# Performance work log

Hardware: AMD Instinct MI355X
Metric: run time of the kernel (lower is better)

Reference implementation:

```python
import jax, jax.numpy as jnp
import numpy as np
from jax import lax

B, T, D = 2048, 300, 40
H = 64          # BasicLSTMCell num_units
D1 = 128        # dense1 units
OUT = 512       # out_dim (num speakers)
FORGET_BIAS = 1.0
BN_EPS = 1e-3   # tf.layers.BatchNormalization default


def setup_inputs() -> dict:
    key = jax.random.key(0)
    ks = jax.random.split(key, 10)
    X = jax.random.normal(ks[0], (B, T, D), dtype=jnp.float32)
    seq_length = jax.random.randint(ks[1], (B,), 1, T + 1).astype(jnp.int32)
    # BasicLSTMCell kernel: [input_dim + H, 4H], gate order i, j, f, o
    lstm_kernel = jax.random.normal(ks[2], (D + H, 4 * H), dtype=jnp.float32) * 0.08
    lstm_bias = jnp.zeros((4 * H,), dtype=jnp.float32)
    W1 = jax.random.normal(ks[3], (H, D1), dtype=jnp.float32) * 0.1
    b1 = jnp.zeros((D1,), dtype=jnp.float32)
    gamma = jnp.ones((D1,), dtype=jnp.float32)
    beta = jnp.zeros((D1,), dtype=jnp.float32)
    moving_mean = jnp.zeros((D1,), dtype=jnp.float32)
    moving_var = jnp.ones((D1,), dtype=jnp.float32)
    W2 = jax.random.normal(ks[4], (D1, OUT), dtype=jnp.float32) * 0.1
    b2 = jnp.zeros((OUT,), dtype=jnp.float32)
    return {"X": X, "seq_length": seq_length,
            "lstm_kernel": lstm_kernel, "lstm_bias": lstm_bias,
            "W1": W1, "b1": b1, "gamma": gamma, "beta": beta,
            "moving_mean": moving_mean, "moving_var": moving_var,
            "W2": W2, "b2": b2}


def reference(X, seq_length, lstm_kernel, lstm_bias, W1, b1, gamma, beta,
              moving_mean, moving_var, W2, b2):
    b = X.shape[0]
    c0 = jnp.zeros((b, H), dtype=X.dtype)
    h0 = jnp.zeros((b, H), dtype=X.dtype)

    def step(carry, x_t):
        c, h = carry
        z = jnp.concatenate([x_t, h], axis=1) @ lstm_kernel + lstm_bias
        i, j, f, o = jnp.split(z, 4, axis=1)
        new_c = c * jax.nn.sigmoid(f + FORGET_BIAS) + jax.nn.sigmoid(i) * jnp.tanh(j)
        new_h = jnp.tanh(new_c) * jax.nn.sigmoid(o)
        return (new_c, new_h), new_h

    _, outs = lax.scan(step, (c0, h0), jnp.swapaxes(X, 0, 1))  # [T, B, H]
    outs = jnp.swapaxes(outs, 0, 1)  # [B, T, H]

    # gather last valid timestep per sample
    idx = (seq_length - 1).astype(jnp.int32)
    final = jnp.take_along_axis(outs, idx[:, None, None], axis=1)[:, 0, :]  # [B, H]

    x = jax.nn.relu(final @ W1 + b1)
    # BatchNorm in inference mode (training=False): use moving statistics
    x = gamma * (x - moving_mean) * lax.rsqrt(moving_var + BN_EPS) + beta
    return jax.nn.softmax(x @ W2 + b2, axis=-1)
```

## Files before the change

### kernel.cpp

```cpp
#include <hip/hip_runtime.h>
#include <stdint.h>

#define TT 300
#define DD 40
#define SB 8
#define AROW 200
#define ABUF (16 * AROW)

typedef __attribute__((ext_vector_type(8))) short short8;
typedef __attribute__((ext_vector_type(4))) float f32x4;

__device__ __forceinline__ ushort f2bf(float f) {
  uint32_t b = __float_as_uint(f);
  b += 0x7FFFu + ((b >> 16) & 1u);
  return (ushort)(b >> 16);
}

__global__ __launch_bounds__(256, 1) void lstm_mfma_kernel(
    const float* __restrict__ X, const int* __restrict__ seqlen,
    const float* __restrict__ Wk, const float* __restrict__ bias,
    float* __restrict__ hfin)
{
  __shared__ ushort wstage[64 * 192];
  __shared__ ushort Ash[2 * ABUF];

  const int tid = threadIdx.x;
  const int wv = tid >> 6, lane = tid & 63;
  const int s0 = blockIdx.x * SB;

  for (int i = tid; i < 2 * ABUF; i += 256) Ash[i] = 0;

  short8 Bf[6][4];
  for (int c = 0; c < 4; ++c) {
    __syncthreads();
    for (int i = tid; i < 64 * 192; i += 256) {
      int cc = i & 63, kp = i >> 6;
      int g = cc >> 4, u = c * 16 + (cc & 15);
      int col = g * 64 + u;
      ushort v = 0;
      if (kp < 40) {
        v = f2bf(Wk[kp * 256 + col]);
      } else if (kp < 42) {
        float bv = bias[col] + ((g == 2) ? 1.0f : 0.0f);
        ushort hi = f2bf(bv);
        v = (kp == 40) ? hi : f2bf(bv - __uint_as_float((uint32_t)hi << 16));
      } else if (kp >= 64) {
        v = f2bf(Wk[(40 + ((kp - 64) >> 1)) * 256 + col]);
      }
      wstage[cc * 192 + kp] = v;
    }
    __syncthreads();
    if (wv == c) {
      #pragma unroll
      for (int kt = 0; kt < 6; ++kt) {
        int kk = kt * 32 + (lane >> 4) * 8;
        #pragma unroll
        for (int g = 0; g < 4; ++g)
          Bf[kt][g] = *reinterpret_cast<const short8*>(
              &wstage[(g * 16 + (lane & 15)) * 192 + kk]);
      }
    }
  }

  const int u = wv * 16 + (lane & 15);
  const int q = lane >> 4;
  const int sl0 = 2 * q, sl1 = sl0 + 1;
  const int len0 = seqlen[s0 + sl0], len1 = seqlen[s0 + sl1];

  int ml = seqlen[s0 + (lane & 7)];
  #pragma unroll
  for (int off = 1; off < 8; off <<= 1) ml = max(ml, __shfl_xor(ml, off));

  const int iA = tid, iB = 256 + tid;
  const int sA = (iA * 205) >> 13, dA = iA - sA * 40;
  int sB = (iB * 205) >> 13; if (sB > 7) sB = 7;
  const int dB = iB - sB * 40;
  const int rA = 4 * (sA >> 1) + (sA & 1), rB = 4 * (sB >> 1) + (sB & 1);
  const float* pA = X + (size_t)(s0 + sA) * (TT * DD) + dA;
  const float* pB = X + (size_t)(s0 + sB) * (TT * DD) + dB;
  const bool hasB = (iB < SB * DD);
  const int xiA = rA * AROW + dA, xiB = rB * AROW + dB;

  if (tid < 16) {
    int s = tid & 7, b = tid >> 3;
    int row = 4 * (s >> 1) + (s & 1);
    Ash[b * ABUF + row * AROW + 40] = 0x3F80;
    Ash[b * ABUF + row * AROW + 41] = 0x3F80;
  }
  Ash[xiA] = f2bf(pA[0]);
  if (hasB) Ash[xiB] = f2bf(pB[0]);
  __syncthreads();
  pA += DD; pB += DD;

  float c0 = 0.f, c1 = 0.f, hf0 = 0.f, hf1 = 0.f;
  int rb = 0, wb = ABUF;
  const int afb = (lane & 15) * AROW + q * 8;
  const int hw0 = (q * 4) * AROW + 64 + 2 * u;
  const int hw1 = (q * 4 + 1) * AROW + 64 + 2 * u;

  for (int t = 0; t < ml; ++t) {
    short8 Af[6];
    #pragma unroll
    for (int kt = 0; kt < 6; ++kt)
      Af[kt] = *reinterpret_cast<const short8*>(&Ash[rb + afb + kt * 32]);

    const bool pre = (t + 1 < ml);
    float xnA = 0.f, xnB = 0.f;
    if (pre) {
      xnA = pA[0]; pA += DD;
      if (hasB) { xnB = pB[0]; pB += DD; }
    }

    f32x4 zero4 = {0.f, 0.f, 0.f, 0.f};
    f32x4 acc0 = zero4, acc1 = zero4, acc2 = zero4, acc3 = zero4;
    #pragma unroll
    for (int kt = 0; kt < 6; ++kt) {
      acc0 = __builtin_amdgcn_mfma_f32_16x16x32_bf16(Af[kt], Bf[kt][0], acc0, 0, 0, 0);
      acc1 = __builtin_amdgcn_mfma_f32_16x16x32_bf16(Af[kt], Bf[kt][1], acc1, 0, 0, 0);
      acc2 = __builtin_amdgcn_mfma_f32_16x16x32_bf16(Af[kt], Bf[kt][2], acc2, 0, 0, 0);
      acc3 = __builtin_amdgcn_mfma_f32_16x16x32_bf16(Af[kt], Bf[kt][3], acc3, 0, 0, 0);
    }

    float Ef0 = __expf(-acc2[0]), Ei0 = __expf(-acc0[0]), Ej0 = __expf(2.f * acc1[0]);
    float nc0 = fmaf(c0, __builtin_amdgcn_rcpf(1.f + Ef0),
                     (Ej0 - 1.f) * __builtin_amdgcn_rcpf((1.f + Ei0) * (1.f + Ej0)));
    float En0 = __expf(2.f * fminf(nc0, 44.f)), Eo0 = __expf(-acc3[0]);
    float nh0 = (En0 - 1.f) * __builtin_amdgcn_rcpf((1.f + En0) * (1.f + Eo0));

    float Ef1 = __expf(-acc2[1]), Ei1 = __expf(-acc0[1]), Ej1 = __expf(2.f * acc1[1]);
    float nc1 = fmaf(c1, __builtin_amdgcn_rcpf(1.f + Ef1),
                     (Ej1 - 1.f) * __builtin_amdgcn_rcpf((1.f + Ei1) * (1.f + Ej1)));
    float En1 = __expf(2.f * fminf(nc1, 44.f)), Eo1 = __expf(-acc3[1]);
    float nh1 = (En1 - 1.f) * __builtin_amdgcn_rcpf((1.f + En1) * (1.f + Eo1));

    c0 = nc0; c1 = nc1;
    if (t == len0 - 1) hf0 = nh0;
    if (t == len1 - 1) hf1 = nh1;

    ushort hh0 = f2bf(nh0);
    ushort hl0 = f2bf(nh0 - __uint_as_float((uint32_t)hh0 << 16));
    ushort hh1 = f2bf(nh1);
    ushort hl1 = f2bf(nh1 - __uint_as_float((uint32_t)hh1 << 16));
    *reinterpret_cast<uint32_t*>(&Ash[wb + hw0]) = (uint32_t)hh0 | ((uint32_t)hl0 << 16);
    *reinterpret_cast<uint32_t*>(&Ash[wb + hw1]) = (uint32_t)hh1 | ((uint32_t)hl1 << 16);
    if (pre) {
      Ash[wb + xiA] = f2bf(xnA);
      if (hasB) Ash[wb + xiB] = f2bf(xnB);
    }
    __syncthreads();
    rb ^= ABUF; wb ^= ABUF;
  }

  hfin[(size_t)(s0 + sl0) * 64 + u] = hf0;
  hfin[(size_t)(s0 + sl1) * 64 + u] = hf1;
}

__global__ __launch_bounds__(256, 1) void head_kernel(
    const float* __restrict__ hfin,
    const float* __restrict__ W1, const float* __restrict__ b1,
    const float* __restrict__ gamma, const float* __restrict__ beta,
    const float* __restrict__ mmean, const float* __restrict__ mvar,
    const float* __restrict__ W2, const float* __restrict__ b2,
    float* __restrict__ out)
{
  __shared__ float hl[16 * 64];
  __shared__ float d1t[128 * 20];
  __shared__ float lg[16 * 516];
  const int tid = threadIdx.x;
  const int b0 = blockIdx.x * 16;

  for (int i = tid; i < 16 * 64; i += 256) hl[i] = hfin[(size_t)b0 * 64 + i];
  __syncthreads();

  {
    const int j = tid & 127, sg = tid >> 7;
    float acc[8];
    const float bb = b1[j];
    #pragma unroll
    for (int s = 0; s < 8; ++s) acc[s] = bb;
    for (int k = 0; k < 64; ++k) {
      float w = W1[k * 128 + j];
      #pragma unroll
      for (int s = 0; s < 8; ++s) acc[s] = fmaf(hl[(sg * 8 + s) * 64 + k], w, acc[s]);
    }
    const float ga = gamma[j], be = beta[j], mm = mmean[j];
    const float iv = rsqrtf(mvar[j] + 1e-3f);
    #pragma unroll
    for (int s = 0; s < 8; ++s) {
      float v = fmaxf(acc[s], 0.f);
      d1t[j * 20 + sg * 8 + s] = ga * (v - mm) * iv + be;
    }
  }
  __syncthreads();

  {
    const int cA = tid * 2;
    float accA[16], accB[16];
    const float bA = b2[cA], bB = b2[cA + 1];
    #pragma unroll
    for (int s = 0; s < 16; ++s) { accA[s] = bA; accB[s] = bB; }
    for (int k = 0; k < 128; ++k) {
      const float2 w = *reinterpret_cast<const float2*>(&W2[k * 512 + cA]);
      const f32x4 dq0 = *reinterpret_cast<const f32x4*>(&d1t[k * 20]);
      const f32x4 dq1 = *reinterpret_cast<const f32x4*>(&d1t[k * 20 + 4]);
      const f32x4 dq2 = *reinterpret_cast<const f32x4*>(&d1t[k * 20 + 8]);
      const f32x4 dq3 = *reinterpret_cast<const f32x4*>(&d1t[k * 20 + 12]);
      #pragma unroll
      for (int s = 0; s < 4; ++s) {
        accA[s]      = fmaf(dq0[s], w.x, accA[s]);      accB[s]      = fmaf(dq0[s], w.y, accB[s]);
        accA[s + 4]  = fmaf(dq1[s], w.x, accA[s + 4]);  accB[s + 4]  = fmaf(dq1[s], w.y, accB[s + 4]);
        accA[s + 8]  = fmaf(dq2[s], w.x, accA[s + 8]);  accB[s + 8]  = fmaf(dq2[s], w.y, accB[s + 8]);
        accA[s + 12] = fmaf(dq3[s], w.x, accA[s + 12]); accB[s + 12] = fmaf(dq3[s], w.y, accB[s + 12]);
      }
    }
    #pragma unroll
    for (int s = 0; s < 16; ++s) {
      lg[s * 516 + cA]     = accA[s];
      lg[s * 516 + cA + 1] = accB[s];
    }
  }
  __syncthreads();

  {
    const int w = tid >> 6, lane = tid & 63;
    #pragma unroll
    for (int si = 0; si < 4; ++si) {
      const int s = w * 4 + si;
      float v[8];
      float m = -3.4e38f;
      #pragma unroll
      for (int i = 0; i < 8; ++i) { v[i] = lg[s * 516 + lane + 64 * i]; m = fmaxf(m, v[i]); }
      #pragma unroll
      for (int off = 1; off < 64; off <<= 1) m = fmaxf(m, __shfl_xor(m, off));
      float sum = 0.f;
      #pragma unroll
      for (int i = 0; i < 8; ++i) { v[i] = __expf(v[i] - m); sum += v[i]; }
      #pragma unroll
      for (int off = 1; off < 64; off <<= 1) sum += __shfl_xor(sum, off);
      const float inv = __builtin_amdgcn_rcpf(sum);
      #pragma unroll
      for (int i = 0; i < 8; ++i)
        out[(size_t)(b0 + s) * 512 + lane + 64 * i] = v[i] * inv;
    }
  }
}

extern "C" void kernel_launch(void* const* d_in, const int* in_sizes, int n_in,
                              void* d_out, int out_size, void* d_ws, size_t ws_size,
                              hipStream_t stream) {
  const float* X      = (const float*)d_in[0];
  const int*   seqlen = (const int*)d_in[1];
  const float* Wk     = (const float*)d_in[2];
  const float* bias   = (const float*)d_in[3];
  const float* W1     = (const float*)d_in[4];
  const float* b1     = (const float*)d_in[5];
  const float* gam    = (const float*)d_in[6];
  const float* bet    = (const float*)d_in[7];
  const float* mmean  = (const float*)d_in[8];
  const float* mvar   = (const float*)d_in[9];
  const float* W2     = (const float*)d_in[10];
  const float* b2     = (const float*)d_in[11];
  float* out  = (float*)d_out;
  float* hfin = (float*)d_ws;

  lstm_mfma_kernel<<<dim3(256), dim3(256), 0, stream>>>(X, seqlen, Wk, bias, hfin);
  head_kernel<<<dim3(128), dim3(256), 0, stream>>>(hfin, W1, b1, gam, bet,
                                                   mmean, mvar, W2, b2, out);
}
```

Measured before the change: 407.8 us.

## Halve per-block batch to 4 samples, doubling LSTM blocks, and add X prefetch distance

Each LSTM block now handles 4 sequences instead of 8, so the grid doubles to 512 blocks and spreads over more compute units on the MI355X. Only half the lanes run the gate math and write h, while X loads are issued two steps ahead and held in a register to hide global latency. The __syncthreads is replaced by a custom barrier that waits only on LDS counters, so global prefetches are not drained each step. MFMA work per step is unchanged and half of its rows are now padding, so per-sample efficiency drops in exchange for more parallelism.

```diff
diff --git a/kernel.cpp b/kernel.cpp
--- a/kernel.cpp
+++ b/kernel.cpp
@@ -3,7 +3,7 @@
 
 #define TT 300
 #define DD 40
-#define SB 8
+#define SB 4
 #define AROW 200
 #define ABUF (16 * AROW)
 
@@ -14,6 +14,12 @@
   uint32_t b = __float_as_uint(f);
   b += 0x7FFFu + ((b >> 16) & 1u);
   return (ushort)(b >> 16);
+}
+
+__device__ __forceinline__ void bar() {
+  asm volatile("s_waitcnt lgkmcnt(0)" ::: "memory");
+  __builtin_amdgcn_s_barrier();
+  asm volatile("" ::: "memory");
 }
 
 __global__ __launch_bounds__(256, 1) void lstm_mfma_kernel(
@@ -64,33 +70,33 @@
 
   const int u = wv * 16 + (lane & 15);
   const int q = lane >> 4;
+  const bool act = (q < 2);
   const int sl0 = 2 * q, sl1 = sl0 + 1;
-  const int len0 = seqlen[s0 + sl0], len1 = seqlen[s0 + sl1];
-
-  int ml = seqlen[s0 + (lane & 7)];
+  const int len0 = seqlen[s0 + (sl0 & 3)], len1 = seqlen[s0 + (sl1 & 3)];
+
+  int ml = seqlen[s0 + (lane & 3)];
   #pragma unroll
-  for (int off = 1; off < 8; off <<= 1) ml = max(ml, __shfl_xor(ml, off));
-
-  const int iA = tid, iB = 256 + tid;
-  const int sA = (iA * 205) >> 13, dA = iA - sA * 40;
-  int sB = (iB * 205) >> 13; if (sB > 7) sB = 7;
-  const int dB = iB - sB * 40;
-  const int rA = 4 * (sA >> 1) + (sA & 1), rB = 4 * (sB >> 1) + (sB & 1);
+  for (int off = 1; off < 4; off <<= 1) ml = max(ml, __shfl_xor(ml, off));
+
+  const bool hasX = (tid < SB * DD);
+  const int sA = (tid * 205) >> 13, dA = tid - sA * 40;
+  const int rA = 4 * (sA >> 1) + (sA & 1);
   const float* pA = X + (size_t)(s0 + sA) * (TT * DD) + dA;
-  const float* pB = X + (size_t)(s0 + sB) * (TT * DD) + dB;
-  const bool hasB = (iB < SB * DD);
-  const int xiA = rA * AROW + dA, xiB = rB * AROW + dB;
-
-  if (tid < 16) {
-    int s = tid & 7, b = tid >> 3;
+  const int xiA = rA * AROW + dA;
+
+  if (tid < 8) {
+    int s = tid & 3, b = tid >> 2;
     int row = 4 * (s >> 1) + (s & 1);
     Ash[b * ABUF + row * AROW + 40] = 0x3F80;
     Ash[b * ABUF + row * AROW + 41] = 0x3F80;
   }
-  Ash[xiA] = f2bf(pA[0]);
-  if (hasB) Ash[xiB] = f2bf(pB[0]);
-  __syncthreads();
-  pA += DD; pB += DD;
+  float xv = 0.f;
+  if (hasX) {
+    Ash[xiA] = f2bf(pA[0]);
+    if (ml > 1) xv = pA[DD];
+  }
+  __syncthreads();
+  pA += 2 * DD;
 
   float c0 = 0.f, c1 = 0.f, hf0 = 0.f, hf1 = 0.f;
   int rb = 0, wb = ABUF;
@@ -104,12 +110,8 @@
     for (int kt = 0; kt < 6; ++kt)
       Af[kt] = *reinterpret_cast<const short8*>(&Ash[rb + afb + kt * 32]);
 
-    const bool pre = (t + 1 < ml);
-    float xnA = 0.f, xnB = 0.f;
-    if (pre) {
-      xnA = pA[0]; pA += DD;
-      if (hasB) { xnB = pB[0]; pB += DD; }
-    }
+    float xn = 0.f;
+    if (hasX && t + 2 < ml) { xn = pA[0]; pA += DD; }
 
     f32x4 zero4 = {0.f, 0.f, 0.f, 0.f};
     f32x4 acc0 = zero4, acc1 = zero4, acc2 = zero4, acc3 = zero4;
@@ -121,38 +123,41 @@
       acc3 = __builtin_amdgcn_mfma_f32_16x16x32_bf16(Af[kt], Bf[kt][3], acc3, 0, 0, 0);
     }
 
-    float Ef0 = __expf(-acc2[0]), Ei0 = __expf(-acc0[0]), Ej0 = __expf(2.f * acc1[0]);
-    float nc0 = fmaf(c0, __builtin_amdgcn_rcpf(1.f + Ef0),
-                     (Ej0 - 1.f) * __builtin_amdgcn_rcpf((1.f + Ei0) * (1.f + Ej0)));
-    float En0 = __expf(2.f * fminf(nc0, 44.f)), Eo0 = __expf(-acc3[0]);
-    float nh0 = (En0 - 1.f) * __builtin_amdgcn_rcpf((1.f + En0) * (1.f + Eo0));
-
-    float Ef1 = __expf(-acc2[1]), Ei1 = __expf(-acc0[1]), Ej1 = __expf(2.f * acc1[1]);
-    float nc1 = fmaf(c1, __builtin_amdgcn_rcpf(1.f + Ef1),
-                     (Ej1 - 1.f) * __builtin_amdgcn_rcpf((1.f + Ei1) * (1.f + Ej1)));
-    float En1 = __expf(2.f * fminf(nc1, 44.f)), Eo1 = __expf(-acc3[1]);
-    float nh1 = (En1 - 1.f) * __builtin_amdgcn_rcpf((1.f + En1) * (1.f + Eo1));
-
-    c0 = nc0; c1 = nc1;
-    if (t == len0 - 1) hf0 = nh0;
-    if (t == len1 - 1) hf1 = nh1;
-
-    ushort hh0 = f2bf(nh0);
-    ushort hl0 = f2bf(nh0 - __uint_as_float((uint32_t)hh0 << 16));
-    ushort hh1 = f2bf(nh1);
-    ushort hl1 = f2bf(nh1 - __uint_as_float((uint32_t)hh1 << 16));
-    *reinterpret_cast<uint32_t*>(&Ash[wb + hw0]) = (uint32_t)hh0 | ((uint32_t)hl0 << 16);
-    *reinterpret_cast<uint32_t*>(&Ash[wb + hw1]) = (uint32_t)hh1 | ((uint32_t)hl1 << 16);
-    if (pre) {
-      Ash[wb + xiA] = f2bf(xnA);
-      if (hasB) Ash[wb + xiB] = f2bf(xnB);
-    }
-    __syncthreads();
+    if (act) {
+      float Ef0 = __expf(-acc2[0]), Ei0 = __expf(-acc0[0]), Ej0 = __expf(2.f * acc1[0]);
+      float nc0 = fmaf(c0, __builtin_amdgcn_rcpf(1.f + Ef0),
+                       (Ej0 - 1.f) * __builtin_amdgcn_rcpf((1.f + Ei0) * (1.f + Ej0)));
+      float En0 = __expf(2.f * fminf(nc0, 44.f)), Eo0 = __expf(-acc3[0]);
+      float nh0 = (En0 - 1.f) * __builtin_amdgcn_rcpf((1.f + En0) * (1.f + Eo0));
+
+      float Ef1 = __expf(-acc2[1]), Ei1 = __expf(-acc0[1]), Ej1 = __expf(2.f * acc1[1]);
+      float nc1 = fmaf(c1, __builtin_amdgcn_rcpf(1.f + Ef1),
+                       (Ej1 - 1.f) * __builtin_amdgcn_rcpf((1.f + Ei1) * (1.f + Ej1)));
+      float En1 = __expf(2.f * fminf(nc1, 44.f)), Eo1 = __expf(-acc3[1]);
+      float nh1 = (En1 - 1.f) * __builtin_amdgcn_rcpf((1.f + En1) * (1.f + Eo1));
+
+      c0 = nc0; c1 = nc1;
+      if (t == len0 - 1) hf0 = nh0;
+      if (t == len1 - 1) hf1 = nh1;
+
+      ushort hh0 = f2bf(nh0);
+      ushort hl0 = f2bf(nh0 - __uint_as_float((uint32_t)hh0 << 16));
+      ushort hh1 = f2bf(nh1);
+      ushort hl1 = f2bf(nh1 - __uint_as_float((uint32_t)hh1 << 16));
+      *reinterpret_cast<uint32_t*>(&Ash[wb + hw0]) = (uint32_t)hh0 | ((uint32_t)hl0 << 16);
+      *reinterpret_cast<uint32_t*>(&Ash[wb + hw1]) = (uint32_t)hh1 | ((uint32_t)hl1 << 16);
+    }
+    if (hasX && t + 1 < ml) Ash[wb + xiA] = f2bf(xv);
+
+    bar();
     rb ^= ABUF; wb ^= ABUF;
-  }
-
-  hfin[(size_t)(s0 + sl0) * 64 + u] = hf0;
-  hfin[(size_t)(s0 + sl1) * 64 + u] = hf1;
+    xv = xn;
+  }
+
+  if (act) {
+    hfin[(size_t)(s0 + sl0) * 64 + u] = hf0;
+    hfin[(size_t)(s0 + sl1) * 64 + u] = hf1;
+  }
 }
 
 __global__ __launch_bounds__(256, 1) void head_kernel(
@@ -263,7 +268,7 @@
   float* out  = (float*)d_out;
   float* hfin = (float*)d_ws;
 
-  lstm_mfma_kernel<<<dim3(256), dim3(256), 0, stream>>>(X, seqlen, Wk, bias, hfin);
+  lstm_mfma_kernel<<<dim3(2048 / SB), dim3(256), 0, stream>>>(X, seqlen, Wk, bias, hfin);
   head_kernel<<<dim3(128), dim3(256), 0, stream>>>(hfin, W1, b1, gam, bet,
                                                    mmean, mvar, W2, b2, out);
 }
```

Result: slower. 425.7 us (+4.4%).

## Split recurrent and input MFMAs, prefetch X two steps ahead, lighter barrier

Applied to the files above, without the earlier changes.

The per-step GEMM is split into the h-dependent part and the x-dependent part, so the x-input MFMAs and X stores can overlap with the recurrent work. X is now prefetched two timesteps ahead, so global load latency is hidden across a full step. The weight staging buffer is aliased with the A buffers to reduce LDS use, and the __syncthreads is replaced by a barrier that waits only on LDS counters, so in-flight global loads are not drained. The hi part of the bf16 split for h now uses truncation instead of rounding, which saves a few ALU ops and stays exact because the lo part holds the remainder.

```diff
diff --git a/kernel.cpp b/kernel.cpp
--- a/kernel.cpp
+++ b/kernel.cpp
@@ -16,23 +16,26 @@
   return (ushort)(b >> 16);
 }
 
+__device__ __forceinline__ void bar() {
+  asm volatile("s_waitcnt lgkmcnt(0)" ::: "memory");
+  __builtin_amdgcn_s_barrier();
+  asm volatile("" ::: "memory");
+}
+
 __global__ __launch_bounds__(256, 1) void lstm_mfma_kernel(
     const float* __restrict__ X, const int* __restrict__ seqlen,
     const float* __restrict__ Wk, const float* __restrict__ bias,
     float* __restrict__ hfin)
 {
-  __shared__ ushort wstage[64 * 192];
-  __shared__ ushort Ash[2 * ABUF];
+  __shared__ ushort shmem[64 * 192];
+  ushort* const Ash = shmem;
 
   const int tid = threadIdx.x;
   const int wv = tid >> 6, lane = tid & 63;
   const int s0 = blockIdx.x * SB;
 
-  for (int i = tid; i < 2 * ABUF; i += 256) Ash[i] = 0;
-
   short8 Bf[6][4];
   for (int c = 0; c < 4; ++c) {
-    __syncthreads();
     for (int i = tid; i < 64 * 192; i += 256) {
       int cc = i & 63, kp = i >> 6;
       int g = cc >> 4, u = c * 16 + (cc & 15);
@@ -47,7 +50,7 @@
       } else if (kp >= 64) {
         v = f2bf(Wk[(40 + ((kp - 64) >> 1)) * 256 + col]);
       }
-      wstage[cc * 192 + kp] = v;
+      shmem[cc * 192 + kp] = v;
     }
     __syncthreads();
     if (wv == c) {
@@ -57,10 +60,13 @@
         #pragma unroll
         for (int g = 0; g < 4; ++g)
           Bf[kt][g] = *reinterpret_cast<const short8*>(
-              &wstage[(g * 16 + (lane & 15)) * 192 + kk]);
+              &shmem[(g * 16 + (lane & 15)) * 192 + kk]);
       }
     }
-  }
+    __syncthreads();
+  }
+
+  for (int i = tid; i < 2 * ABUF; i += 256) Ash[i] = 0;
 
   const int u = wv * 16 + (lane & 15);
   const int q = lane >> 4;
@@ -89,8 +95,13 @@
   }
   Ash[xiA] = f2bf(pA[0]);
   if (hasB) Ash[xiB] = f2bf(pB[0]);
-  __syncthreads();
-  pA += DD; pB += DD;
+  float xvA = 0.f, xvB = 0.f;
+  if (ml > 1) {
+    xvA = pA[DD];
+    if (hasB) xvB = pB[DD];
+  }
+  __syncthreads();
+  pA += 2 * DD; pB += 2 * DD;
 
   float c0 = 0.f, c1 = 0.f, hf0 = 0.f, hf1 = 0.f;
   int rb = 0, wb = ABUF;
@@ -99,56 +110,72 @@
   const int hw1 = (q * 4 + 1) * AROW + 64 + 2 * u;
 
   for (int t = 0; t < ml; ++t) {
-    short8 Af[6];
-    #pragma unroll
-    for (int kt = 0; kt < 6; ++kt)
-      Af[kt] = *reinterpret_cast<const short8*>(&Ash[rb + afb + kt * 32]);
-
-    const bool pre = (t + 1 < ml);
+    short8 Ah[4];
+    #pragma unroll
+    for (int k2 = 0; k2 < 4; ++k2)
+      Ah[k2] = *reinterpret_cast<const short8*>(&Ash[rb + afb + (k2 + 2) * 32]);
+
+    f32x4 zero4 = {0.f, 0.f, 0.f, 0.f};
+    f32x4 ah0 = zero4, ah1 = zero4, ah2 = zero4, ah3 = zero4;
+    #pragma unroll
+    for (int k2 = 0; k2 < 4; ++k2) {
+      ah0 = __builtin_amdgcn_mfma_f32_16x16x32_bf16(Ah[k2], Bf[k2 + 2][0], ah0, 0, 0, 0);
+      ah1 = __builtin_amdgcn_mfma_f32_16x16x32_bf16(Ah[k2], Bf[k2 + 2][1], ah1, 0, 0, 0);
+      ah2 = __builtin_amdgcn_mfma_f32_16x16x32_bf16(Ah[k2], Bf[k2 + 2][2], ah2, 0, 0, 0);
+      ah3 = __builtin_amdgcn_mfma_f32_16x16x32_bf16(Ah[k2], Bf[k2 + 2][3], ah3, 0, 0, 0);
+    }
+
+    short8 Ax[2];
+    #pragma unroll
+    for (int k2 = 0; k2 < 2; ++k2)
+      Ax[k2] = *reinterpret_cast<const short8*>(&Ash[rb + afb + k2 * 32]);
+
+    if (t + 1 < ml) {
+      Ash[wb + xiA] = f2bf(xvA);
+      if (hasB) Ash[wb + xiB] = f2bf(xvB);
+    }
     float xnA = 0.f, xnB = 0.f;
-    if (pre) {
+    if (t + 2 < ml) {
       xnA = pA[0]; pA += DD;
       if (hasB) { xnB = pB[0]; pB += DD; }
     }
 
-    f32x4 zero4 = {0.f, 0.f, 0.f, 0.f};
-    f32x4 acc0 = zero4, acc1 = zero4, acc2 = zero4, acc3 = zero4;
-    #pragma unroll
-    for (int kt = 0; kt < 6; ++kt) {
-      acc0 = __builtin_amdgcn_mfma_f32_16x16x32_bf16(Af[kt], Bf[kt][0], acc0, 0, 0, 0);
-      acc1 = __builtin_amdgcn_mfma_f32_16x16x32_bf16(Af[kt], Bf[kt][1], acc1, 0, 0, 0);
-      acc2 = __builtin_amdgcn_mfma_f32_16x16x32_bf16(Af[kt], Bf[kt][2], acc2, 0, 0, 0);
-      acc3 = __builtin_amdgcn_mfma_f32_16x16x32_bf16(Af[kt], Bf[kt][3], acc3, 0, 0, 0);
-    }
-
-    float Ef0 = __expf(-acc2[0]), Ei0 = __expf(-acc0[0]), Ej0 = __expf(2.f * acc1[0]);
+    f32x4 ax0 = zero4, ax1 = zero4, ax2 = zero4, ax3 = zero4;
+    #pragma unroll
+    for (int k2 = 0; k2 < 2; ++k2) {
+      ax0 = __builtin_amdgcn_mfma_f32_16x16x32_bf16(Ax[k2], Bf[k2][0], ax0, 0, 0, 0);
+      ax1 = __builtin_amdgcn_mfma_f32_16x16x32_bf16(Ax[k2], Bf[k2][1], ax1, 0, 0, 0);
+      ax2 = __builtin_amdgcn_mfma_f32_16x16x32_bf16(Ax[k2], Bf[k2][2], ax2, 0, 0, 0);
+      ax3 = __builtin_amdgcn_mfma_f32_16x16x32_bf16(Ax[k2], Bf[k2][3], ax3, 0, 0, 0);
+    }
+    f32x4 z0 = ah0 + ax0, z1 = ah1 + ax1, z2 = ah2 + ax2, z3 = ah3 + ax3;
+
+    float Ef0 = __expf(-z2[0]), Ei0 = __expf(-z0[0]), Ej0 = __expf(2.f * z1[0]);
     float nc0 = fmaf(c0, __builtin_amdgcn_rcpf(1.f + Ef0),
                      (Ej0 - 1.f) * __builtin_amdgcn_rcpf((1.f + Ei0) * (1.f + Ej0)));
-    float En0 = __expf(2.f * fminf(nc0, 44.f)), Eo0 = __expf(-acc3[0]);
+    float En0 = __expf(2.f * fminf(nc0, 44.f)), Eo0 = __expf(-z3[0]);
     float nh0 = (En0 - 1.f) * __builtin_amdgcn_rcpf((1.f + En0) * (1.f + Eo0));
 
-    float Ef1 = __expf(-acc2[1]), Ei1 = __expf(-acc0[1]), Ej1 = __expf(2.f * acc1[1]);
+    float Ef1 = __expf(-z2[1]), Ei1 = __expf(-z0[1]), Ej1 = __expf(2.f * z1[1]);
     float nc1 = fmaf(c1, __builtin_amdgcn_rcpf(1.f + Ef1),
                      (Ej1 - 1.f) * __builtin_amdgcn_rcpf((1.f + Ei1) * (1.f + Ej1)));
-    float En1 = __expf(2.f * fminf(nc1, 44.f)), Eo1 = __expf(-acc3[1]);
+    float En1 = __expf(2.f * fminf(nc1, 44.f)), Eo1 = __expf(-z3[1]);
     float nh1 = (En1 - 1.f) * __builtin_amdgcn_rcpf((1.f + En1) * (1.f + Eo1));
 
     c0 = nc0; c1 = nc1;
     if (t == len0 - 1) hf0 = nh0;
     if (t == len1 - 1) hf1 = nh1;
 
-    ushort hh0 = f2bf(nh0);
+    ushort hh0 = (ushort)(__float_as_uint(nh0) >> 16);
     ushort hl0 = f2bf(nh0 - __uint_as_float((uint32_t)hh0 << 16));
-    ushort hh1 = f2bf(nh1);
+    ushort hh1 = (ushort)(__float_as_uint(nh1) >> 16);
     ushort hl1 = f2bf(nh1 - __uint_as_float((uint32_t)hh1 << 16));
     *reinterpret_cast<uint32_t*>(&Ash[wb + hw0]) = (uint32_t)hh0 | ((uint32_t)hl0 << 16);
     *reinterpret_cast<uint32_t*>(&Ash[wb + hw1]) = (uint32_t)hh1 | ((uint32_t)hl1 << 16);
-    if (pre) {
-      Ash[wb + xiA] = f2bf(xnA);
-      if (hasB) Ash[wb + xiB] = f2bf(xnB);
-    }
-    __syncthreads();
+
+    bar();
     rb ^= ABUF; wb ^= ABUF;
+    xvA = xnA; xvB = xnB;
   }
 
   hfin[(size_t)(s0 + sl0) * 64 + u] = hf0;
@@ -263,7 +290,7 @@
   float* out  = (float*)d_out;
   float* hfin = (float*)d_ws;
 
-  lstm_mfma_kernel<<<dim3(256), dim3(256), 0, stream>>>(X, seqlen, Wk, bias, hfin);
+  lstm_mfma_kernel<<<dim3(2048 / SB), dim3(256), 0, stream>>>(X, seqlen, Wk, bias, hfin);
   head_kernel<<<dim3(128), dim3(256), 0, stream>>>(hfin, W1, b1, gam, bet,
                                                    mmean, mvar, W2, b2, out);
 }
```

Measured after the change: 398.1 us. 1.02x faster.
